# Optimization experiments

Hardware: AMD Instinct MI355X
Metric: run time of the kernel (lower is better)

The kernel has to match this reference:

```python
import jax, jax.numpy as jnp
import numpy as np

N_NODES = 50000
N_EDGES = 800000
D_NODE = 128
D_EDGE = 128
D_HID = 128
D_OUT = 128


def setup_inputs() -> dict:
    key = jax.random.key(0)
    ks = jax.random.split(key, 6)
    d_in = 2 * D_NODE + D_EDGE  # 384
    return {
        "cell_attr": jax.random.normal(ks[0], (N_NODES, D_NODE), dtype=jnp.float32),
        "edge_attr": jax.random.normal(ks[1], (N_EDGES, D_EDGE), dtype=jnp.float32),
        "W1": jax.random.normal(ks[2], (d_in, D_HID), dtype=jnp.float32) * (1.0 / np.sqrt(d_in)),
        "b1": jnp.zeros((D_HID,), dtype=jnp.float32),
        "W2": jax.random.normal(ks[3], (D_HID, D_OUT), dtype=jnp.float32) * (1.0 / np.sqrt(D_HID)),
        "b2": jnp.zeros((D_OUT,), dtype=jnp.float32),
        "edge_index": jax.random.randint(ks[4], (2, N_EDGES), 0, N_NODES, dtype=jnp.int64) if jax.config.jax_enable_x64 else jax.random.randint(ks[4], (2, N_EDGES), 0, N_NODES, dtype=jnp.int32),
    }


def reference(cell_attr, edge_attr, W1, b1, W2, b2, edge_index):
    # Gather sender/receiver node features via edge_index: [E, d_node] each
    senders_attr = cell_attr[edge_index[0]]
    receivers_attr = cell_attr[edge_index[1]]
    # Concat -> [E, 2*d_node + d_edge]
    collected = jnp.concatenate([senders_attr, receivers_attr, edge_attr], axis=1)
    # MLP (custom_func): Linear -> ReLU -> Linear
    h = jax.nn.relu(collected @ W1 + b1)
    edge_attr_new = h @ W2 + b2
    return edge_attr_new
```

## Files before the change

### kernel.cpp

```cpp
#include <hip/hip_runtime.h>
#include <stdint.h>

#define D 128
#define K1 384
#define TM 64
#define N_EDGES 800000
#define N_NODES 50000

typedef __attribute__((ext_vector_type(8))) short short8;
typedef __attribute__((ext_vector_type(4))) float f32x4;
typedef unsigned int u32;

__device__ __forceinline__ u32 bf16_rne(float f) {
    u32 u = __builtin_bit_cast(u32, f);
    return (u + 0x7FFFu + ((u >> 16) & 1u)) >> 16;
}
__device__ __forceinline__ u32 pk2(float lo, float hi) {
    return bf16_rne(lo) | (bf16_rne(hi) << 16);
}

__device__ __forceinline__ void gl_lds16(const void* g, void* l) {
    __builtin_amdgcn_global_load_lds(
        (const __attribute__((address_space(1))) void*)g,
        (__attribute__((address_space(3))) void*)l,
        16, 0, 0);
}

__global__ void prep_cell(const float* __restrict__ src, unsigned short* __restrict__ dst, int n4) {
    int i = blockIdx.x * blockDim.x + threadIdx.x;
    if (i >= n4) return;
    float4 v = ((const float4*)src)[i];
    ushort4 o;
    o.x = (unsigned short)bf16_rne(v.x);
    o.y = (unsigned short)bf16_rne(v.y);
    o.z = (unsigned short)bf16_rne(v.z);
    o.w = (unsigned short)bf16_rne(v.w);
    ((ushort4*)dst)[i] = o;
}

__global__ void prep_w(const float* __restrict__ W1, const float* __restrict__ W2,
                       unsigned short* __restrict__ W1F, unsigned short* __restrict__ W2F) {
    int id = blockIdx.x * blockDim.x + threadIdx.x;
    if (id < K1 * D) {
        int k = id >> 7, n = id & 127;
        int c = k >> 7, kr = k & 127;
        int kk = kr >> 5, qq = (kr >> 3) & 3, e = k & 7;
        int TN = n >> 4, l16 = n & 15;
        int seg = ((c * 4 + kk) * 8 + TN) * 64 + qq * 16 + l16;
        W1F[seg * 8 + e] = (unsigned short)bf16_rne(W1[id]);
    } else {
        int id2 = id - K1 * D;
        int k = id2 >> 7, n = id2 & 127;
        int kk = k >> 5, qq = (k >> 3) & 3, e = k & 7;
        int TN = n >> 4, l16 = n & 15;
        int seg = (kk * 8 + TN) * 64 + qq * 16 + l16;
        W2F[seg * 8 + e] = (unsigned short)bf16_rne(W2[id2]);
    }
}

template <bool CELL_BF16>
__global__ __launch_bounds__(256, 4) void edge_mlp(
    const float* __restrict__ cell_f32,
    const unsigned short* __restrict__ cellb,
    const float* __restrict__ edge_attr,
    const unsigned short* __restrict__ W1F,
    const float* __restrict__ b1,
    const unsigned short* __restrict__ W2F,
    const float* __restrict__ b2,
    const int* __restrict__ sidx,
    const int* __restrict__ ridx,
    float* __restrict__ out)
{
    __shared__ __align__(16) unsigned short sA[2][TM * D];

    const int tid  = threadIdx.x;
    const int lane = tid & 63;
    const int wave = tid >> 6;
    const int l16  = lane & 15;
    const int q    = lane >> 4;
    const int e0   = blockIdx.x * TM;
    const int rb   = tid >> 4;
    const int seg  = tid & 15;

    auto stage_cell = [&](const int* __restrict__ idxp, unsigned short* buf) {
        if constexpr (CELL_BF16) {
#pragma unroll
            for (int it = 0; it < 4; ++it) {
                const int row = it * 16 + wave * 4 + q;
                const int node = idxp[e0 + row];
                const int srcoff = (l16 ^ (row & 7)) * 8;
                gl_lds16(cellb + (size_t)node * D + srcoff,
                         (char*)buf + wave * 1024 + it * 4096);
            }
        } else {
#pragma unroll
            for (int it = 0; it < 4; ++it) {
                const int row = rb + it * 16;
                const int node = idxp[e0 + row];
                const float* src = cell_f32 + (size_t)node * D + seg * 8;
                float4 f0 = *(const float4*)src;
                float4 f1 = *(const float4*)(src + 4);
                uint4 v = make_uint4(pk2(f0.x, f0.y), pk2(f0.z, f0.w),
                                     pk2(f1.x, f1.y), pk2(f1.z, f1.w));
                *(uint4*)((char*)buf + row * 256 + ((seg ^ (row & 7)) * 16)) = v;
            }
        }
    };

    short8 wf[4][2];
    auto load_w1 = [&](int c) {
#pragma unroll
        for (int kk = 0; kk < 4; ++kk)
#pragma unroll
            for (int nt = 0; nt < 2; ++nt)
                wf[kk][nt] = *(const short8*)(W1F +
                    (size_t)(((c * 4 + kk) * 8 + wave * 2 + nt) * 64 + lane) * 8);
    };

    f32x4 acc[4][2];
#pragma unroll
    for (int i = 0; i < 4; ++i)
#pragma unroll
        for (int j = 0; j < 2; ++j) acc[i][j] = (f32x4){0.f, 0.f, 0.f, 0.f};

    auto compute_chunk = [&](const unsigned short* buf) {
#pragma unroll
        for (int kk = 0; kk < 4; ++kk)
#pragma unroll
            for (int mt = 0; mt < 4; ++mt) {
                const int row = mt * 16 + l16;
                short8 a = *(const short8*)((const char*)buf + row * 256 +
                                            (((kk * 4 + q) ^ (row & 7)) * 16));
                acc[mt][0] = __builtin_amdgcn_mfma_f32_16x16x32_bf16(wf[kk][0], a, acc[mt][0], 0, 0, 0);
                acc[mt][1] = __builtin_amdgcn_mfma_f32_16x16x32_bf16(wf[kk][1], a, acc[mt][1], 0, 0, 0);
            }
    };

    stage_cell(sidx, sA[0]);
    __syncthreads();

    load_w1(0);
    stage_cell(ridx, sA[1]);
    compute_chunk(sA[0]);
    __syncthreads();

    load_w1(1);
    float4 ef0[4], ef1[4];
#pragma unroll
    for (int it = 0; it < 4; ++it) {
        const float* src = edge_attr + (size_t)(e0 + rb + it * 16) * D + seg * 8;
        ef0[it] = *(const float4*)src;
        ef1[it] = *(const float4*)(src + 4);
    }
    compute_chunk(sA[1]);
#pragma unroll
    for (int it = 0; it < 4; ++it) {
        const int row = rb + it * 16;
        uint4 v = make_uint4(pk2(ef0[it].x, ef0[it].y), pk2(ef0[it].z, ef0[it].w),
                             pk2(ef1[it].x, ef1[it].y), pk2(ef1[it].z, ef1[it].w));
        *(uint4*)((char*)sA[0] + row * 256 + ((seg ^ (row & 7)) * 16)) = v;
    }
    __syncthreads();

    load_w1(2);
    compute_chunk(sA[0]);

    short8 w2f[4][2];
#pragma unroll
    for (int kk = 0; kk < 4; ++kk)
#pragma unroll
        for (int nt = 0; nt < 2; ++nt)
            w2f[kk][nt] = *(const short8*)(W2F +
                (size_t)((kk * 8 + wave * 2 + nt) * 64 + lane) * 8);

    f32x4 b1v[2];
#pragma unroll
    for (int nt = 0; nt < 2; ++nt)
        b1v[nt] = *(const f32x4*)(b1 + wave * 32 + nt * 16 + q * 4);

#pragma unroll
    for (int mt = 0; mt < 4; ++mt)
#pragma unroll
        for (int nt = 0; nt < 2; ++nt) {
            f32x4 v = acc[mt][nt] + b1v[nt];
#pragma unroll
            for (int r = 0; r < 4; ++r) v[r] = v[r] > 0.f ? v[r] : 0.f;
            const int M = mt * 16 + l16;
            const int slot = (wave * 4 + nt * 2 + (q >> 1)) ^ (M & 7);
            *(uint2*)((char*)sA[1] + M * 256 + slot * 16 + (q & 1) * 8) =
                make_uint2(pk2(v[0], v[1]), pk2(v[2], v[3]));
        }
    __syncthreads();

    f32x4 acc2[4][2];
#pragma unroll
    for (int i = 0; i < 4; ++i)
#pragma unroll
        for (int j = 0; j < 2; ++j) acc2[i][j] = (f32x4){0.f, 0.f, 0.f, 0.f};

#pragma unroll
    for (int kk = 0; kk < 4; ++kk)
#pragma unroll
        for (int mt = 0; mt < 4; ++mt) {
            const int row = mt * 16 + l16;
            short8 h = *(const short8*)((const char*)sA[1] + row * 256 +
                                        (((kk * 4 + q) ^ (row & 7)) * 16));
            acc2[mt][0] = __builtin_amdgcn_mfma_f32_16x16x32_bf16(w2f[kk][0], h, acc2[mt][0], 0, 0, 0);
            acc2[mt][1] = __builtin_amdgcn_mfma_f32_16x16x32_bf16(w2f[kk][1], h, acc2[mt][1], 0, 0, 0);
        }

    f32x4 b2v[2];
#pragma unroll
    for (int nt = 0; nt < 2; ++nt)
        b2v[nt] = *(const f32x4*)(b2 + wave * 32 + nt * 16 + q * 4);

#pragma unroll
    for (int mt = 0; mt < 4; ++mt)
#pragma unroll
        for (int nt = 0; nt < 2; ++nt) {
            f32x4 o = acc2[mt][nt] + b2v[nt];
            *(f32x4*)(out + (size_t)(e0 + mt * 16 + l16) * D + wave * 32 + nt * 16 + q * 4) = o;
        }
}

extern "C" void kernel_launch(void* const* d_in, const int* in_sizes, int n_in,
                              void* d_out, int out_size, void* d_ws, size_t ws_size,
                              hipStream_t stream) {
    const float* cell = (const float*)d_in[0];
    const float* edge = (const float*)d_in[1];
    const float* W1   = (const float*)d_in[2];
    const float* b1   = (const float*)d_in[3];
    const float* W2   = (const float*)d_in[4];
    const float* b2   = (const float*)d_in[5];
    const int*   eidx = (const int*)d_in[6];

    const size_t cell_bytes = (size_t)N_NODES * D * 2;
    const size_t w1f_bytes  = (size_t)K1 * D * 2;
    const size_t w2f_bytes  = (size_t)D * D * 2;

    bool cell_in_ws = ws_size >= cell_bytes + w1f_bytes + w2f_bytes;
    unsigned short* cellb;
    unsigned short* W1F;
    if (cell_in_ws) {
        cellb = (unsigned short*)d_ws;
        W1F   = (unsigned short*)((char*)d_ws + cell_bytes);
    } else {
        cellb = nullptr;
        W1F   = (unsigned short*)d_ws;
    }
    unsigned short* W2F = W1F + K1 * D;

    if (cell_in_ws) {
        int n4 = N_NODES * D / 4;
        prep_cell<<<(n4 + 255) / 256, 256, 0, stream>>>(cell, cellb, n4);
    }
    prep_w<<<(K1 * D + D * D) / 256, 256, 0, stream>>>(W1, W2, W1F, W2F);

    const int* sidx = eidx;
    const int* ridx = eidx + N_EDGES;
    if (cell_in_ws) {
        edge_mlp<true><<<N_EDGES / TM, 256, 0, stream>>>(
            cell, cellb, edge, W1F, b1, W2F, b2, sidx, ridx, (float*)d_out);
    } else {
        edge_mlp<false><<<N_EDGES / TM, 256, 0, stream>>>(
            cell, cellb, edge, W1F, b1, W2F, b2, sidx, ridx, (float*)d_out);
    }
}
```

Measured before the change: 770.0 us.

## Convert edge MLP to persistent grid with cross-tile gather prefetch

The kernel becomes persistent: 1024 blocks loop over the 12500 edge tiles instead of launching one block per tile. The next tile's sender rows are DMA'd into LDS during the second GEMM, and its index loads are issued early, so gather latency overlaps compute. W2 fragments now reuse the W1 registers to keep register pressure down. The risk is tail imbalance, since the tile count is not divisible by the grid, and less latency hiding from block-level parallelism when only about 4 blocks run per CU.

```diff
diff --git a/kernel.cpp b/kernel.cpp
--- a/kernel.cpp
+++ b/kernel.cpp
@@ -6,6 +6,8 @@
 #define TM 64
 #define N_EDGES 800000
 #define N_NODES 50000
+#define NT (N_EDGES / TM)
+#define GRID 1024
 
 typedef __attribute__((ext_vector_type(8))) short short8;
 typedef __attribute__((ext_vector_type(4))) float f32x4;
@@ -71,39 +73,42 @@
     const int* __restrict__ ridx,
     float* __restrict__ out)
 {
-    __shared__ __align__(16) unsigned short sA[2][TM * D];
+    __shared__ __align__(16) unsigned short bA[TM * D];
+    __shared__ __align__(16) unsigned short bB[TM * D];
 
     const int tid  = threadIdx.x;
     const int lane = tid & 63;
     const int wave = tid >> 6;
     const int l16  = lane & 15;
     const int q    = lane >> 4;
-    const int e0   = blockIdx.x * TM;
     const int rb   = tid >> 4;
     const int seg  = tid & 15;
 
-    auto stage_cell = [&](const int* __restrict__ idxp, unsigned short* buf) {
-        if constexpr (CELL_BF16) {
-#pragma unroll
-            for (int it = 0; it < 4; ++it) {
-                const int row = it * 16 + wave * 4 + q;
-                const int node = idxp[e0 + row];
-                const int srcoff = (l16 ^ (row & 7)) * 8;
-                gl_lds16(cellb + (size_t)node * D + srcoff,
-                         (char*)buf + wave * 1024 + it * 4096);
-            }
-        } else {
-#pragma unroll
-            for (int it = 0; it < 4; ++it) {
-                const int row = rb + it * 16;
-                const int node = idxp[e0 + row];
-                const float* src = cell_f32 + (size_t)node * D + seg * 8;
-                float4 f0 = *(const float4*)src;
-                float4 f1 = *(const float4*)(src + 4);
-                uint4 v = make_uint4(pk2(f0.x, f0.y), pk2(f0.z, f0.w),
-                                     pk2(f1.x, f1.y), pk2(f1.z, f1.w));
-                *(uint4*)((char*)buf + row * 256 + ((seg ^ (row & 7)) * 16)) = v;
-            }
+    auto dma_cell = [&](const int* nidx, unsigned short* buf) {
+#pragma unroll
+        for (int it = 0; it < 4; ++it) {
+            const int row = it * 16 + wave * 4 + q;
+            const int srcoff = (l16 ^ (row & 7)) * 8;
+            gl_lds16(cellb + (size_t)nidx[it] * D + srcoff,
+                     (char*)buf + wave * 1024 + it * 4096);
+        }
+    };
+    auto load_idx = [&](const int* __restrict__ idxp, int e0s, int* nidx) {
+#pragma unroll
+        for (int it = 0; it < 4; ++it)
+            nidx[it] = idxp[e0s + it * 16 + wave * 4 + q];
+    };
+    auto stage_f32 = [&](const int* __restrict__ idxp, int e0s, unsigned short* buf) {
+#pragma unroll
+        for (int it = 0; it < 4; ++it) {
+            const int row = rb + it * 16;
+            const int node = idxp[e0s + row];
+            const float* src = cell_f32 + (size_t)node * D + seg * 8;
+            float4 f0 = *(const float4*)src;
+            float4 f1 = *(const float4*)(src + 4);
+            uint4 v = make_uint4(pk2(f0.x, f0.y), pk2(f0.z, f0.w),
+                                 pk2(f1.x, f1.y), pk2(f1.z, f1.w));
+            *(uint4*)((char*)buf + row * 256 + ((seg ^ (row & 7)) * 16)) = v;
         }
     };
 
@@ -116,13 +121,22 @@
                 wf[kk][nt] = *(const short8*)(W1F +
                     (size_t)(((c * 4 + kk) * 8 + wave * 2 + nt) * 64 + lane) * 8);
     };
+    auto load_w2 = [&]() {
+#pragma unroll
+        for (int kk = 0; kk < 4; ++kk)
+#pragma unroll
+            for (int nt = 0; nt < 2; ++nt)
+                wf[kk][nt] = *(const short8*)(W2F +
+                    (size_t)((kk * 8 + wave * 2 + nt) * 64 + lane) * 8);
+    };
 
     f32x4 acc[4][2];
-#pragma unroll
-    for (int i = 0; i < 4; ++i)
-#pragma unroll
-        for (int j = 0; j < 2; ++j) acc[i][j] = (f32x4){0.f, 0.f, 0.f, 0.f};
-
+    auto zero_acc = [&]() {
+#pragma unroll
+        for (int i = 0; i < 4; ++i)
+#pragma unroll
+            for (int j = 0; j < 2; ++j) acc[i][j] = (f32x4){0.f, 0.f, 0.f, 0.f};
+    };
     auto compute_chunk = [&](const unsigned short* buf) {
 #pragma unroll
         for (int kk = 0; kk < 4; ++kk)
@@ -136,91 +150,122 @@
             }
     };
 
-    stage_cell(sidx, sA[0]);
+    f32x4 b1v[2], b2v[2];
+#pragma unroll
+    for (int nt = 0; nt < 2; ++nt) {
+        b1v[nt] = *(const f32x4*)(b1 + wave * 32 + nt * 16 + q * 4);
+        b2v[nt] = *(const f32x4*)(b2 + wave * 32 + nt * 16 + q * 4);
+    }
+
+    int t = blockIdx.x;
+    if (t >= NT) return;
+
+    int nidxS[4], nidxR[4];
+    if constexpr (CELL_BF16) {
+        load_idx(sidx, t * TM, nidxS);
+        dma_cell(nidxS, bA);
+        load_idx(ridx, t * TM, nidxR);
+    } else {
+        stage_f32(sidx, t * TM, bA);
+    }
+    load_w1(0);
     __syncthreads();
 
-    load_w1(0);
-    stage_cell(ridx, sA[1]);
-    compute_chunk(sA[0]);
-    __syncthreads();
-
-    load_w1(1);
-    float4 ef0[4], ef1[4];
-#pragma unroll
-    for (int it = 0; it < 4; ++it) {
-        const float* src = edge_attr + (size_t)(e0 + rb + it * 16) * D + seg * 8;
-        ef0[it] = *(const float4*)src;
-        ef1[it] = *(const float4*)(src + 4);
-    }
-    compute_chunk(sA[1]);
-#pragma unroll
-    for (int it = 0; it < 4; ++it) {
-        const int row = rb + it * 16;
-        uint4 v = make_uint4(pk2(ef0[it].x, ef0[it].y), pk2(ef0[it].z, ef0[it].w),
-                             pk2(ef1[it].x, ef1[it].y), pk2(ef1[it].z, ef1[it].w));
-        *(uint4*)((char*)sA[0] + row * 256 + ((seg ^ (row & 7)) * 16)) = v;
-    }
-    __syncthreads();
-
-    load_w1(2);
-    compute_chunk(sA[0]);
-
-    short8 w2f[4][2];
-#pragma unroll
-    for (int kk = 0; kk < 4; ++kk)
-#pragma unroll
-        for (int nt = 0; nt < 2; ++nt)
-            w2f[kk][nt] = *(const short8*)(W2F +
-                (size_t)((kk * 8 + wave * 2 + nt) * 64 + lane) * 8);
-
-    f32x4 b1v[2];
-#pragma unroll
-    for (int nt = 0; nt < 2; ++nt)
-        b1v[nt] = *(const f32x4*)(b1 + wave * 32 + nt * 16 + q * 4);
-
-#pragma unroll
-    for (int mt = 0; mt < 4; ++mt)
-#pragma unroll
-        for (int nt = 0; nt < 2; ++nt) {
-            f32x4 v = acc[mt][nt] + b1v[nt];
-#pragma unroll
-            for (int r = 0; r < 4; ++r) v[r] = v[r] > 0.f ? v[r] : 0.f;
-            const int M = mt * 16 + l16;
-            const int slot = (wave * 4 + nt * 2 + (q >> 1)) ^ (M & 7);
-            *(uint2*)((char*)sA[1] + M * 256 + slot * 16 + (q & 1) * 8) =
-                make_uint2(pk2(v[0], v[1]), pk2(v[2], v[3]));
-        }
-    __syncthreads();
-
-    f32x4 acc2[4][2];
-#pragma unroll
-    for (int i = 0; i < 4; ++i)
-#pragma unroll
-        for (int j = 0; j < 2; ++j) acc2[i][j] = (f32x4){0.f, 0.f, 0.f, 0.f};
-
-#pragma unroll
-    for (int kk = 0; kk < 4; ++kk)
-#pragma unroll
-        for (int mt = 0; mt < 4; ++mt) {
-            const int row = mt * 16 + l16;
-            short8 h = *(const short8*)((const char*)sA[1] + row * 256 +
-                                        (((kk * 4 + q) ^ (row & 7)) * 16));
-            acc2[mt][0] = __builtin_amdgcn_mfma_f32_16x16x32_bf16(w2f[kk][0], h, acc2[mt][0], 0, 0, 0);
-            acc2[mt][1] = __builtin_amdgcn_mfma_f32_16x16x32_bf16(w2f[kk][1], h, acc2[mt][1], 0, 0, 0);
-        }
-
-    f32x4 b2v[2];
-#pragma unroll
-    for (int nt = 0; nt < 2; ++nt)
-        b2v[nt] = *(const f32x4*)(b2 + wave * 32 + nt * 16 + q * 4);
-
-#pragma unroll
-    for (int mt = 0; mt < 4; ++mt)
-#pragma unroll
-        for (int nt = 0; nt < 2; ++nt) {
-            f32x4 o = acc2[mt][nt] + b2v[nt];
-            *(f32x4*)(out + (size_t)(e0 + mt * 16 + l16) * D + wave * 32 + nt * 16 + q * 4) = o;
-        }
+    for (;;) {
+        const int e0 = t * TM;
+        const int tn = t + GRID;
+        const bool more = tn < NT;
+        zero_acc();
+
+        if constexpr (CELL_BF16) dma_cell(nidxR, bB);
+        else                     stage_f32(ridx, e0, bB);
+        float4 ef[8];
+#pragma unroll
+        for (int it = 0; it < 2; ++it) {
+            const float* src = edge_attr + (size_t)(e0 + rb + it * 16) * D + seg * 8;
+            ef[it * 2]     = *(const float4*)src;
+            ef[it * 2 + 1] = *(const float4*)(src + 4);
+        }
+        compute_chunk(bA);
+        load_w1(1);
+        __syncthreads();
+
+#pragma unroll
+        for (int it = 2; it < 4; ++it) {
+            const float* src = edge_attr + (size_t)(e0 + rb + it * 16) * D + seg * 8;
+            ef[it * 2]     = *(const float4*)src;
+            ef[it * 2 + 1] = *(const float4*)(src + 4);
+        }
+        uint4 evA[2];
+#pragma unroll
+        for (int it = 0; it < 2; ++it)
+            evA[it] = make_uint4(pk2(ef[it*2].x, ef[it*2].y),   pk2(ef[it*2].z, ef[it*2].w),
+                                 pk2(ef[it*2+1].x, ef[it*2+1].y), pk2(ef[it*2+1].z, ef[it*2+1].w));
+        compute_chunk(bB);
+#pragma unroll
+        for (int it = 0; it < 2; ++it) {
+            const int row = rb + it * 16;
+            *(uint4*)((char*)bA + row * 256 + ((seg ^ (row & 7)) * 16)) = evA[it];
+        }
+#pragma unroll
+        for (int it = 2; it < 4; ++it) {
+            const int row = rb + it * 16;
+            uint4 v = make_uint4(pk2(ef[it*2].x, ef[it*2].y),   pk2(ef[it*2].z, ef[it*2].w),
+                                 pk2(ef[it*2+1].x, ef[it*2+1].y), pk2(ef[it*2+1].z, ef[it*2+1].w));
+            *(uint4*)((char*)bA + row * 256 + ((seg ^ (row & 7)) * 16)) = v;
+        }
+        load_w1(2);
+        __syncthreads();
+
+        compute_chunk(bA);
+        if (more) {
+            if constexpr (CELL_BF16) load_idx(sidx, tn * TM, nidxS);
+        }
+#pragma unroll
+        for (int mt = 0; mt < 4; ++mt)
+#pragma unroll
+            for (int nt = 0; nt < 2; ++nt) {
+                f32x4 v = acc[mt][nt] + b1v[nt];
+#pragma unroll
+                for (int r = 0; r < 4; ++r) v[r] = v[r] > 0.f ? v[r] : 0.f;
+                const int M = mt * 16 + l16;
+                const int slot = (wave * 4 + nt * 2 + (q >> 1)) ^ (M & 7);
+                *(uint2*)((char*)bB + M * 256 + slot * 16 + (q & 1) * 8) =
+                    make_uint2(pk2(v[0], v[1]), pk2(v[2], v[3]));
+            }
+        load_w2();
+        __syncthreads();
+
+        if (more) {
+            if constexpr (CELL_BF16) dma_cell(nidxS, bA);
+            else                     stage_f32(sidx, tn * TM, bA);
+        }
+        zero_acc();
+#pragma unroll
+        for (int kk = 0; kk < 4; ++kk)
+#pragma unroll
+            for (int mt = 0; mt < 4; ++mt) {
+                const int row = mt * 16 + l16;
+                short8 h = *(const short8*)((const char*)bB + row * 256 +
+                                            (((kk * 4 + q) ^ (row & 7)) * 16));
+                acc[mt][0] = __builtin_amdgcn_mfma_f32_16x16x32_bf16(wf[kk][0], h, acc[mt][0], 0, 0, 0);
+                acc[mt][1] = __builtin_amdgcn_mfma_f32_16x16x32_bf16(wf[kk][1], h, acc[mt][1], 0, 0, 0);
+            }
+        if (more) {
+            if constexpr (CELL_BF16) load_idx(ridx, tn * TM, nidxR);
+        }
+#pragma unroll
+        for (int mt = 0; mt < 4; ++mt)
+#pragma unroll
+            for (int nt = 0; nt < 2; ++nt) {
+                f32x4 o = acc[mt][nt] + b2v[nt];
+                *(f32x4*)(out + (size_t)(e0 + mt * 16 + l16) * D + wave * 32 + nt * 16 + q * 4) = o;
+            }
+        if (more) load_w1(0);
+        __syncthreads();
+        if (!more) break;
+        t = tn;
+    }
 }
 
 extern "C" void kernel_launch(void* const* d_in, const int* in_sizes, int n_in,
@@ -259,10 +304,10 @@
     const int* sidx = eidx;
     const int* ridx = eidx + N_EDGES;
     if (cell_in_ws) {
-        edge_mlp<true><<<N_EDGES / TM, 256, 0, stream>>>(
+        edge_mlp<true><<<GRID, 256, 0, stream>>>(
             cell, cellb, edge, W1F, b1, W2F, b2, sidx, ridx, (float*)d_out);
     } else {
-        edge_mlp<false><<<N_EDGES / TM, 256, 0, stream>>>(
+        edge_mlp<false><<<GRID, 256, 0, stream>>>(
             cell, cellb, edge, W1F, b1, W2F, b2, sidx, ridx, (float*)d_out);
     }
 }
```

New measurement: 1.046 ms. 35.9% more time.
